# Kernel optimization log

Hardware: AMD Instinct MI355X
Metric: run time of the kernel (lower is better)

Reference implementation:

```python
import jax, jax.numpy as jnp
import numpy as np

NUM_LAYERS = 4
HIDDEN = 32
INPUT = 2
B = 16384
T = 64


def setup_inputs() -> dict:
    key = jax.random.key(0)
    ks = jax.random.split(key, 8)
    s = 1.0 / np.sqrt(HIDDEN)  # PyTorch LSTM default init scale
    return {
        "x": jax.random.normal(ks[0], (B, 3, T), dtype=jnp.float32),
        "W_ih0": jax.random.uniform(ks[1], (4 * HIDDEN, INPUT), minval=-s, maxval=s, dtype=jnp.float32),
        "W_ih": jax.random.uniform(ks[2], (NUM_LAYERS - 1, 4 * HIDDEN, HIDDEN), minval=-s, maxval=s, dtype=jnp.float32),
        "W_hh": jax.random.uniform(ks[3], (NUM_LAYERS, 4 * HIDDEN, HIDDEN), minval=-s, maxval=s, dtype=jnp.float32),
        "b_ih": jax.random.uniform(ks[4], (NUM_LAYERS, 4 * HIDDEN), minval=-s, maxval=s, dtype=jnp.float32),
        "b_hh": jax.random.uniform(ks[5], (NUM_LAYERS, 4 * HIDDEN), minval=-s, maxval=s, dtype=jnp.float32),
        "W_lin": jax.random.uniform(ks[6], (1, HIDDEN), minval=-s, maxval=s, dtype=jnp.float32),
        "b_lin": jax.random.uniform(ks[7], (1,), minval=-s, maxval=s, dtype=jnp.float32),
    }


def _lstm_cell(inp, h, c, Wih, Whh, b):
    # inp: [B, in_dim]; h, c: [B, H]; Wih: [4H, in_dim]; Whh: [4H, H]; b: [4H]
    gates = inp @ Wih.T + h @ Whh.T + b  # [B, 4H]
    i, f, g, o = jnp.split(gates, 4, axis=-1)  # PyTorch gate order: i, f, g, o
    i = jax.nn.sigmoid(i)
    f = jax.nn.sigmoid(f)
    g = jnp.tanh(g)
    o = jax.nn.sigmoid(o)
    c_new = f * c + i * g
    h_new = o * jnp.tanh(c_new)
    return h_new, c_new


def reference(x, W_ih0, W_ih, W_hh, b_ih, b_hh, W_lin, b_lin):
    # x: [B, 3, T]; channel 2 (id) is discarded, as in the original forward.
    feats = x[:, :2, :]                         # [B, 2, T]
    xs = jnp.transpose(feats, (2, 0, 1))        # [T, B, 2]
    bsz = x.shape[0]
    h0 = jnp.zeros((NUM_LAYERS, bsz, HIDDEN), dtype=x.dtype)
    c0 = jnp.zeros((NUM_LAYERS, bsz, HIDDEN), dtype=x.dtype)
    bias = b_ih + b_hh  # [L, 4H]

    def step(carry, xt):
        h, c = carry  # each [L, B, H]
        inp = xt
        hs, cs = [], []
        for l in range(NUM_LAYERS):
            Wih = W_ih0 if l == 0 else W_ih[l - 1]
            h_new, c_new = _lstm_cell(inp, h[l], c[l], Wih, W_hh[l], bias[l])
            hs.append(h_new)
            cs.append(c_new)
            inp = h_new
        return (jnp.stack(hs), jnp.stack(cs)), None

    (h, c), _ = jax.lax.scan(step, (h0, c0), xs)
    # last timestep's top-layer output -> linear -> sigmoid -> squeeze to [B]
    out = jax.nn.sigmoid(h[-1] @ W_lin.T + b_lin)  # [B, 1]
    return out.squeeze(-1)
```

## Files before the change

### kernel.cpp

```cpp
#include <hip/hip_runtime.h>

typedef float  f32x4  __attribute__((ext_vector_type(4)));
typedef short  bf16x8 __attribute__((ext_vector_type(8)));

#define LOG2E      1.4426950408889634f
#define NLOG2E    -1.4426950408889634f
#define NTWOLOG2E -2.8853900817779268f

__device__ __forceinline__ unsigned short f2b(float f) {
    unsigned int u = __builtin_bit_cast(unsigned int, f);
    u += 0x7fffu + ((u >> 16) & 1u);
    return (unsigned short)(u >> 16);
}
__device__ __forceinline__ float b2f(unsigned short s) {
    unsigned int u = ((unsigned int)s) << 16;
    return __builtin_bit_cast(float, u);
}
__device__ __forceinline__ unsigned int pk2(float lo, float hi) {
#if __has_builtin(__builtin_amdgcn_cvt_pk_bf16_f32)
    typedef __bf16 bf16x2 __attribute__((ext_vector_type(2)));
    bf16x2 p = __builtin_amdgcn_cvt_pk_bf16_f32(lo, hi);
    return __builtin_bit_cast(unsigned int, p);
#else
    return (unsigned int)f2b(lo) | ((unsigned int)f2b(hi) << 16);
#endif
}
__device__ __forceinline__ float frcp(float x) { return __builtin_amdgcn_rcpf(x); }
__device__ __forceinline__ float fex2(float x) { return __builtin_amdgcn_exp2f(x); }

__global__ __launch_bounds__(256, 2)
void lstm_mfma(const float* __restrict__ xg,  const float* __restrict__ Wih0,
               const float* __restrict__ Wih, const float* __restrict__ Whh,
               const float* __restrict__ bih, const float* __restrict__ bhh,
               const float* __restrict__ Wlin,const float* __restrict__ blin,
               float* __restrict__ out) {
    __shared__ short        hb[16 * 1280] __attribute__((aligned(16)));
    __shared__ unsigned int xb[64 * 32];

    const int tid  = threadIdx.x;
    const int wv   = __builtin_amdgcn_readfirstlane(tid >> 6);
    const int lane = tid & 63;
    const int m    = lane & 15;
    const int q    = lane >> 4;
    const int row0 = blockIdx.x * 32;

    for (int i = tid; i < 10240; i += 256) ((unsigned int*)hb)[i] = 0u;

    for (int i = tid; i < 2048; i += 256) {
        int r = i >> 6, t = i & 63;
        float x0 = xg[(size_t)(row0 + r) * 192 + t];
        float x1 = xg[(size_t)(row0 + r) * 192 + 64 + t];
        xb[t * 32 + r] = pk2(x0, x1);
    }

    bf16x8 bfr[8][2];
    float  bv[8];
#pragma unroll
    for (int g = 0; g < 8; ++g) {
        const int   T    = g >> 1;
        const int   rowG = T * 32 + 2 * m + (g & 1);
        const float sc   = (T == 2) ? NTWOLOG2E : NLOG2E;
        bv[g] = (bih[wv * 128 + rowG] + bhh[wv * 128 + rowG]) * sc;
#pragma unroll
        for (int c = 0; c < 2; ++c) {
            const int k0 = c * 32 + q * 8;
            float w[8];
            if (wv == 0) {
                if (c == 0) {
#pragma unroll
                    for (int jj = 0; jj < 8; ++jj) w[jj] = 0.0f;
                    if (q == 0) { w[0] = Wih0[rowG * 2]; w[1] = Wih0[rowG * 2 + 1]; }
                } else {
                    const float* src = Whh + rowG * 32 + (k0 - 32);
#pragma unroll
                    for (int jj = 0; jj < 8; ++jj) w[jj] = src[jj];
                }
            } else {
                const float* src = (c == 0) ? (Wih + (wv - 1) * 4096 + rowG * 32 + k0)
                                            : (Whh + wv * 4096 + rowG * 32 + (k0 - 32));
#pragma unroll
                for (int jj = 0; jj < 8; ++jj) w[jj] = src[jj];
            }
            bf16x8 fr;
#pragma unroll
            for (int jj = 0; jj < 8; ++jj) fr[jj] = (short)f2b(w[jj] * sc);
            bfr[g][c] = fr;
        }
    }

    float cst[2][2][4];
#pragma unroll
    for (int tt = 0; tt < 2; ++tt)
#pragma unroll
        for (int hf = 0; hf < 2; ++hf)
#pragma unroll
            for (int r = 0; r < 4; ++r) cst[tt][hf][r] = 0.0f;

    __syncthreads();

    auto cell_step = [&](int t, const short* pa0, const short* pa1, short* hwr) {
        bf16x8 a0[2], a1[2];
#pragma unroll
        for (int tt = 0; tt < 2; ++tt) {
            if (wv == 0) {
                unsigned int xd = xb[t * 32 + tt * 16 + m];
                union { unsigned int u[4]; bf16x8 v; } au;
                au.u[0] = (q == 0) ? xd : 0u; au.u[1] = 0u; au.u[2] = 0u; au.u[3] = 0u;
                a0[tt] = au.v;
            } else {
                a0[tt] = *(const bf16x8*)(pa0 + (tt * 16 + m) * 40 + q * 8);
            }
            a1[tt] = *(const bf16x8*)(pa1 + (tt * 16 + m) * 40 + q * 8);
        }
#pragma unroll
        for (int tt = 0; tt < 2; ++tt) {
            f32x4 acc[8];
#pragma unroll
            for (int g = 0; g < 8; ++g) {
                f32x4 cb = {bv[g], bv[g], bv[g], bv[g]};
                acc[g] = __builtin_amdgcn_mfma_f32_16x16x32_bf16(a0[tt], bfr[g][0], cb, 0, 0, 0);
                acc[g] = __builtin_amdgcn_mfma_f32_16x16x32_bf16(a1[tt], bfr[g][1], acc[g], 0, 0, 0);
            }
            float h0[4];
#pragma unroll
            for (int hf = 0; hf < 2; ++hf) {
#pragma unroll
                for (int r = 0; r < 4; ++r) {
                    float ei = fex2(acc[0 + hf][r]);
                    float ef = fex2(acc[2 + hf][r]);
                    float eg = fex2(acc[4 + hf][r]);
                    float eo = fex2(acc[6 + hf][r]);
                    float ap_f = 1.0f + ef;
                    float p1   = (1.0f + ei) * (1.0f + eg);
                    float R    = frcp(p1 * ap_f);
                    float t1   = (1.0f - eg) * ap_f;
                    float t2   = __builtin_fmaf(cst[tt][hf][r], p1, t1);
                    float cn   = t2 * R;
                    cst[tt][hf][r] = cn;
                    float ec = fex2(cn * NTWOLOG2E);
                    float Rh = frcp((1.0f + eo) * (1.0f + ec));
                    float hh = (1.0f - ec) * Rh;
                    if (hf == 0) {
                        h0[r] = hh;
                    } else {
                        ((unsigned int*)hwr)[(tt * 16 + q * 4 + r) * 20 + m] = pk2(h0[r], hh);
                    }
                }
            }
        }
    };

    for (int S = 0; S < 35; ++S) {
        const int t0 = 2 * (S - wv);
        if (t0 >= 0 && t0 <= 62) {
            const int p  = S & 1;
            const int pb = p ^ 1;
            short*       Lc0 = hb + ((wv * 2 + p ) * 2    ) * 1280;
            short*       Lc1 = Lc0 + 1280;
            const short* Lp1 = hb + ((wv * 2 + pb) * 2 + 1) * 1280;
            const int    lb  = (wv > 0) ? (wv - 1) : 0;
            const short* Dp0 = hb + ((lb * 2 + pb) * 2    ) * 1280;
            const short* Dp1 = Dp0 + 1280;

            cell_step(t0,     Dp0, Lp1, Lc0);
            cell_step(t0 + 1, Dp1, Lc0, Lc1);
        }
        __syncthreads();
    }

    if (tid < 32) {
        const short* h3 = hb + ((3 * 2 + 0) * 2 + 1) * 1280;
        float s = blin[0];
#pragma unroll
        for (int k = 0; k < 32; ++k)
            s += Wlin[k] * b2f((unsigned short)h3[tid * 40 + k]);
        out[row0 + tid] = frcp(1.0f + fex2(s * NLOG2E));
    }
}

extern "C" void kernel_launch(void* const* d_in, const int* in_sizes, int n_in,
                              void* d_out, int out_size, void* d_ws, size_t ws_size,
                              hipStream_t stream) {
    const float* x    = (const float*)d_in[0];
    const float* Wih0 = (const float*)d_in[1];
    const float* Wih  = (const float*)d_in[2];
    const float* Whh  = (const float*)d_in[3];
    const float* bih  = (const float*)d_in[4];
    const float* bhh  = (const float*)d_in[5];
    const float* Wlin = (const float*)d_in[6];
    const float* blin = (const float*)d_in[7];
    float* out = (float*)d_out;

    lstm_mfma<<<512, 256, 0, stream>>>(x, Wih0, Wih, Whh, bih, bhh, Wlin, blin, out);
}
```

Measured before the change: 223.7 us.

## Remap waves to layer pairs and row groups, shortening the wavefront pipeline

Instead of one wave per layer handling all 32 rows, each wave now owns two consecutive layers for one 16-row group (pair P, row group Rg). Layers within a pair run back-to-back inside a wave, so the pipeline has two stages instead of four, which cuts the skewed step count from 35 to 33 and needs less shared memory. Each wave now holds weight fragments for two layers, raising register pressure, and the serial chain per step doubles in length. The c-state exponent scaling is also folded into the g-gate FMA.

```diff
diff --git a/kernel.cpp b/kernel.cpp
--- a/kernel.cpp
+++ b/kernel.cpp
@@ -3,7 +3,7 @@
 typedef float  f32x4  __attribute__((ext_vector_type(4)));
 typedef short  bf16x8 __attribute__((ext_vector_type(8)));
 
-#define LOG2E      1.4426950408889634f
+#define TWOLOG2E   2.8853900817779268f
 #define NLOG2E    -1.4426950408889634f
 #define NTWOLOG2E -2.8853900817779268f
 
@@ -34,17 +34,19 @@
                const float* __restrict__ bih, const float* __restrict__ bhh,
                const float* __restrict__ Wlin,const float* __restrict__ blin,
                float* __restrict__ out) {
-    __shared__ short        hb[16 * 1280] __attribute__((aligned(16)));
+    __shared__ short        hb[12800] __attribute__((aligned(16)));
     __shared__ unsigned int xb[64 * 32];
 
     const int tid  = threadIdx.x;
     const int wv   = __builtin_amdgcn_readfirstlane(tid >> 6);
+    const int P    = wv >> 1;
+    const int Rg   = wv & 1;
     const int lane = tid & 63;
     const int m    = lane & 15;
     const int q    = lane >> 4;
     const int row0 = blockIdx.x * 32;
 
-    for (int i = tid; i < 10240; i += 256) ((unsigned int*)hb)[i] = 0u;
+    for (int i = tid; i < 6400; i += 256) ((unsigned int*)hb)[i] = 0u;
 
     for (int i = tid; i < 2048; i += 256) {
         int r = i >> 6, t = i & 63;
@@ -53,127 +55,134 @@
         xb[t * 32 + r] = pk2(x0, x1);
     }
 
-    bf16x8 bfr[8][2];
-    float  bv[8];
-#pragma unroll
-    for (int g = 0; g < 8; ++g) {
-        const int   T    = g >> 1;
-        const int   rowG = T * 32 + 2 * m + (g & 1);
-        const float sc   = (T == 2) ? NTWOLOG2E : NLOG2E;
-        bv[g] = (bih[wv * 128 + rowG] + bhh[wv * 128 + rowG]) * sc;
-#pragma unroll
-        for (int c = 0; c < 2; ++c) {
-            const int k0 = c * 32 + q * 8;
-            float w[8];
-            if (wv == 0) {
-                if (c == 0) {
-#pragma unroll
-                    for (int jj = 0; jj < 8; ++jj) w[jj] = 0.0f;
-                    if (q == 0) { w[0] = Wih0[rowG * 2]; w[1] = Wih0[rowG * 2 + 1]; }
+    bf16x8 bfr[2][8][2];
+    float  bv[2][8];
+#pragma unroll
+    for (int li = 0; li < 2; ++li) {
+        const int l = 2 * P + li;
+#pragma unroll
+        for (int g = 0; g < 8; ++g) {
+            const int   T    = g >> 1;
+            const int   rowG = T * 32 + 2 * m + (g & 1);
+            const float sc   = (T == 2) ? NTWOLOG2E : NLOG2E;
+            bv[li][g] = (bih[l * 128 + rowG] + bhh[l * 128 + rowG]) * sc;
+#pragma unroll
+            for (int c = 0; c < 2; ++c) {
+                const int k0 = c * 32 + q * 8;
+                float w[8];
+                if (l == 0) {
+                    if (c == 0) {
+#pragma unroll
+                        for (int jj = 0; jj < 8; ++jj) w[jj] = 0.0f;
+                        if (q == 0) { w[0] = Wih0[rowG * 2]; w[1] = Wih0[rowG * 2 + 1]; }
+                    } else {
+                        const float* src = Whh + rowG * 32 + (k0 - 32);
+#pragma unroll
+                        for (int jj = 0; jj < 8; ++jj) w[jj] = src[jj];
+                    }
                 } else {
-                    const float* src = Whh + rowG * 32 + (k0 - 32);
+                    const float* src = (c == 0) ? (Wih + (l - 1) * 4096 + rowG * 32 + k0)
+                                                : (Whh + l * 4096 + rowG * 32 + (k0 - 32));
 #pragma unroll
                     for (int jj = 0; jj < 8; ++jj) w[jj] = src[jj];
                 }
-            } else {
-                const float* src = (c == 0) ? (Wih + (wv - 1) * 4096 + rowG * 32 + k0)
-                                            : (Whh + wv * 4096 + rowG * 32 + (k0 - 32));
-#pragma unroll
-                for (int jj = 0; jj < 8; ++jj) w[jj] = src[jj];
+                bf16x8 fr;
+#pragma unroll
+                for (int jj = 0; jj < 8; ++jj) fr[jj] = (short)f2b(w[jj] * sc);
+                bfr[li][g][c] = fr;
             }
-            bf16x8 fr;
-#pragma unroll
-            for (int jj = 0; jj < 8; ++jj) fr[jj] = (short)f2b(w[jj] * sc);
-            bfr[g][c] = fr;
-        }
-    }
-
-    float cst[2][2][4];
-#pragma unroll
-    for (int tt = 0; tt < 2; ++tt)
+        }
+    }
+
+    float cp[2][2][4];
+#pragma unroll
+    for (int li = 0; li < 2; ++li)
 #pragma unroll
         for (int hf = 0; hf < 2; ++hf)
 #pragma unroll
-            for (int r = 0; r < 4; ++r) cst[tt][hf][r] = 0.0f;
+            for (int r = 0; r < 4; ++r) cp[li][hf][r] = 0.0f;
+
+    short* const h0s0 = hb + Rg * 1280;
+    short* const h0s1 = h0s0 + 640;
+    short* const h2s0 = hb + 7680 + Rg * 1280;
+    short* const h2s1 = h2s0 + 640;
+    short* const h3s0 = hb + 10240 + Rg * 1280;
+    short* const h3s1 = h3s0 + 640;
+    auto h1p = [&](int par, int slot) { return hb + 2560 + ((Rg * 2 + par) * 2 + slot) * 640; };
 
     __syncthreads();
 
-    auto cell_step = [&](int t, const short* pa0, const short* pa1, short* hwr) {
-        bf16x8 a0[2], a1[2];
-#pragma unroll
-        for (int tt = 0; tt < 2; ++tt) {
-            if (wv == 0) {
-                unsigned int xd = xb[t * 32 + tt * 16 + m];
-                union { unsigned int u[4]; bf16x8 v; } au;
-                au.u[0] = (q == 0) ? xd : 0u; au.u[1] = 0u; au.u[2] = 0u; au.u[3] = 0u;
-                a0[tt] = au.v;
-            } else {
-                a0[tt] = *(const bf16x8*)(pa0 + (tt * 16 + m) * 40 + q * 8);
+    auto cell = [&](int li, int xt, const short* pinp, const short* prec, short* pwr) {
+        bf16x8 a0, a1;
+        if (P == 0 && li == 0) {
+            unsigned int xd = xb[xt * 32 + Rg * 16 + m];
+            union { unsigned int u[4]; bf16x8 v; } au;
+            au.u[0] = (q == 0) ? xd : 0u; au.u[1] = 0u; au.u[2] = 0u; au.u[3] = 0u;
+            a0 = au.v;
+        } else {
+            a0 = *(const bf16x8*)(pinp + m * 40 + q * 8);
+        }
+        a1 = *(const bf16x8*)(prec + m * 40 + q * 8);
+
+        f32x4 acc[8];
+#pragma unroll
+        for (int g = 0; g < 8; ++g) {
+            f32x4 cb = {bv[li][g], bv[li][g], bv[li][g], bv[li][g]};
+            acc[g] = __builtin_amdgcn_mfma_f32_16x16x32_bf16(a0, bfr[li][g][0], cb, 0, 0, 0);
+            acc[g] = __builtin_amdgcn_mfma_f32_16x16x32_bf16(a1, bfr[li][g][1], acc[g], 0, 0, 0);
+        }
+        float h0v[4];
+#pragma unroll
+        for (int hf = 0; hf < 2; ++hf) {
+#pragma unroll
+            for (int r = 0; r < 4; ++r) {
+                float ei = fex2(acc[0 + hf][r]);
+                float ef = fex2(acc[2 + hf][r]);
+                float eg = fex2(acc[4 + hf][r]);
+                float eo = fex2(acc[6 + hf][r]);
+                float ap_f = 1.0f + ef;
+                float p1   = (1.0f + ei) * (1.0f + eg);
+                float R_   = frcp(p1 * ap_f);
+                float egp  = __builtin_fmaf(eg, TWOLOG2E, NTWOLOG2E);
+                float t1   = egp * ap_f;
+                float t2   = __builtin_fmaf(cp[li][hf][r], p1, t1);
+                float cn   = t2 * R_;
+                cp[li][hf][r] = cn;
+                float ec = fex2(cn);
+                float Rh = frcp((1.0f + eo) * (1.0f + ec));
+                float hh = (1.0f - ec) * Rh;
+                if (hf == 0) h0v[r] = hh;
+                else ((unsigned int*)pwr)[(q * 4 + r) * 20 + m] = pk2(h0v[r], hh);
             }
-            a1[tt] = *(const bf16x8*)(pa1 + (tt * 16 + m) * 40 + q * 8);
-        }
-#pragma unroll
-        for (int tt = 0; tt < 2; ++tt) {
-            f32x4 acc[8];
-#pragma unroll
-            for (int g = 0; g < 8; ++g) {
-                f32x4 cb = {bv[g], bv[g], bv[g], bv[g]};
-                acc[g] = __builtin_amdgcn_mfma_f32_16x16x32_bf16(a0[tt], bfr[g][0], cb, 0, 0, 0);
-                acc[g] = __builtin_amdgcn_mfma_f32_16x16x32_bf16(a1[tt], bfr[g][1], acc[g], 0, 0, 0);
-            }
-            float h0[4];
-#pragma unroll
-            for (int hf = 0; hf < 2; ++hf) {
-#pragma unroll
-                for (int r = 0; r < 4; ++r) {
-                    float ei = fex2(acc[0 + hf][r]);
-                    float ef = fex2(acc[2 + hf][r]);
-                    float eg = fex2(acc[4 + hf][r]);
-                    float eo = fex2(acc[6 + hf][r]);
-                    float ap_f = 1.0f + ef;
-                    float p1   = (1.0f + ei) * (1.0f + eg);
-                    float R    = frcp(p1 * ap_f);
-                    float t1   = (1.0f - eg) * ap_f;
-                    float t2   = __builtin_fmaf(cst[tt][hf][r], p1, t1);
-                    float cn   = t2 * R;
-                    cst[tt][hf][r] = cn;
-                    float ec = fex2(cn * NTWOLOG2E);
-                    float Rh = frcp((1.0f + eo) * (1.0f + ec));
-                    float hh = (1.0f - ec) * Rh;
-                    if (hf == 0) {
-                        h0[r] = hh;
-                    } else {
-                        ((unsigned int*)hwr)[(tt * 16 + q * 4 + r) * 20 + m] = pk2(h0[r], hh);
-                    }
-                }
-            }
         }
     };
 
-    for (int S = 0; S < 35; ++S) {
-        const int t0 = 2 * (S - wv);
+    for (int S = 0; S < 33; ++S) {
+        const int t0 = 2 * (S - P);
         if (t0 >= 0 && t0 <= 62) {
             const int p  = S & 1;
             const int pb = p ^ 1;
-            short*       Lc0 = hb + ((wv * 2 + p ) * 2    ) * 1280;
-            short*       Lc1 = Lc0 + 1280;
-            const short* Lp1 = hb + ((wv * 2 + pb) * 2 + 1) * 1280;
-            const int    lb  = (wv > 0) ? (wv - 1) : 0;
-            const short* Dp0 = hb + ((lb * 2 + pb) * 2    ) * 1280;
-            const short* Dp1 = Dp0 + 1280;
-
-            cell_step(t0,     Dp0, Lp1, Lc0);
-            cell_step(t0 + 1, Dp1, Lc0, Lc1);
+            if (P == 0) {
+                cell(0, t0,     nullptr,    h0s1,       h0s0);
+                cell(0, t0 + 1, nullptr,    h0s0,       h0s1);
+                cell(1, 0,      h0s0,       h1p(pb, 1), h1p(p, 0));
+                cell(1, 0,      h0s1,       h1p(p, 0),  h1p(p, 1));
+            } else {
+                cell(0, 0,      h1p(pb, 0), h2s1,       h2s0);
+                cell(0, 0,      h1p(pb, 1), h2s0,       h2s1);
+                cell(1, 0,      h2s0,       h3s1,       h3s0);
+                cell(1, 0,      h2s1,       h3s0,       h3s1);
+            }
         }
         __syncthreads();
     }
 
     if (tid < 32) {
-        const short* h3 = hb + ((3 * 2 + 0) * 2 + 1) * 1280;
+        const short* h3 = hb + 10240 + (tid >> 4) * 1280 + 640 + (tid & 15) * 40;
         float s = blin[0];
 #pragma unroll
         for (int k = 0; k < 32; ++k)
-            s += Wlin[k] * b2f((unsigned short)h3[tid * 40 + k]);
+            s += Wlin[k] * b2f((unsigned short)h3[k]);
         out[row0 + tid] = frcp(1.0f + fex2(s * NLOG2E));
     }
 }
```

Result: slower. 427.3 us (+91.1%).

## Replace block barriers with per-wave LDS progress flags in layer wavefront pipeline

Applied to the files above, without the earlier changes.

Swaps the lockstep __syncthreads wavefront schedule for point-to-point sync. Each wave, one per layer, spins on LDS progress counters of its upstream and downstream neighbours before each two-step chunk. The hidden-state buffers become a 4-slot ring per layer, so waves can run ahead of each other. The cell math is also adjusted to fold the 2*log2e scaling into the cell state, removing one multiply before exp2. Spin-waiting on volatile LDS with s_sleep risks extra polling overhead, and correctness depends on the ring slot reuse distance and LDS write ordering.

```diff
diff --git a/kernel.cpp b/kernel.cpp
--- a/kernel.cpp
+++ b/kernel.cpp
@@ -3,7 +3,7 @@
 typedef float  f32x4  __attribute__((ext_vector_type(4)));
 typedef short  bf16x8 __attribute__((ext_vector_type(8)));
 
-#define LOG2E      1.4426950408889634f
+#define TWOLOG2E   2.8853900817779268f
 #define NLOG2E    -1.4426950408889634f
 #define NTWOLOG2E -2.8853900817779268f
 
@@ -36,6 +36,7 @@
                float* __restrict__ out) {
     __shared__ short        hb[16 * 1280] __attribute__((aligned(16)));
     __shared__ unsigned int xb[64 * 32];
+    __shared__ int          prog[4];
 
     const int tid  = threadIdx.x;
     const int wv   = __builtin_amdgcn_readfirstlane(tid >> 6);
@@ -45,6 +46,7 @@
     const int row0 = blockIdx.x * 32;
 
     for (int i = tid; i < 10240; i += 256) ((unsigned int*)hb)[i] = 0u;
+    if (tid < 4) prog[tid] = 0;
 
     for (int i = tid; i < 2048; i += 256) {
         int r = i >> 6, t = i & 63;
@@ -88,13 +90,13 @@
         }
     }
 
-    float cst[2][2][4];
+    float cp[2][2][4];
 #pragma unroll
     for (int tt = 0; tt < 2; ++tt)
 #pragma unroll
         for (int hf = 0; hf < 2; ++hf)
 #pragma unroll
-            for (int r = 0; r < 4; ++r) cst[tt][hf][r] = 0.0f;
+            for (int r = 0; r < 4; ++r) cp[tt][hf][r] = 0.0f;
 
     __syncthreads();
 
@@ -132,48 +134,54 @@
                     float eo = fex2(acc[6 + hf][r]);
                     float ap_f = 1.0f + ef;
                     float p1   = (1.0f + ei) * (1.0f + eg);
-                    float R    = frcp(p1 * ap_f);
-                    float t1   = (1.0f - eg) * ap_f;
-                    float t2   = __builtin_fmaf(cst[tt][hf][r], p1, t1);
-                    float cn   = t2 * R;
-                    cst[tt][hf][r] = cn;
-                    float ec = fex2(cn * NTWOLOG2E);
+                    float R_   = frcp(p1 * ap_f);
+                    float egp  = __builtin_fmaf(eg, TWOLOG2E, NTWOLOG2E);
+                    float t1   = egp * ap_f;
+                    float t2   = __builtin_fmaf(cp[tt][hf][r], p1, t1);
+                    float cn   = t2 * R_;
+                    cp[tt][hf][r] = cn;
+                    float ec = fex2(cn);
                     float Rh = frcp((1.0f + eo) * (1.0f + ec));
                     float hh = (1.0f - ec) * Rh;
-                    if (hf == 0) {
-                        h0[r] = hh;
-                    } else {
-                        ((unsigned int*)hwr)[(tt * 16 + q * 4 + r) * 20 + m] = pk2(h0[r], hh);
-                    }
+                    if (hf == 0) h0[r] = hh;
+                    else ((unsigned int*)hwr)[(tt * 16 + q * 4 + r) * 20 + m] = pk2(h0[r], hh);
                 }
             }
         }
     };
 
-    for (int S = 0; S < 35; ++S) {
-        const int t0 = 2 * (S - wv);
-        if (t0 >= 0 && t0 <= 62) {
-            const int p  = S & 1;
-            const int pb = p ^ 1;
-            short*       Lc0 = hb + ((wv * 2 + p ) * 2    ) * 1280;
-            short*       Lc1 = Lc0 + 1280;
-            const short* Lp1 = hb + ((wv * 2 + pb) * 2 + 1) * 1280;
-            const int    lb  = (wv > 0) ? (wv - 1) : 0;
-            const short* Dp0 = hb + ((lb * 2 + pb) * 2    ) * 1280;
-            const short* Dp1 = Dp0 + 1280;
-
-            cell_step(t0,     Dp0, Lp1, Lc0);
-            cell_step(t0 + 1, Dp1, Lc0, Lc1);
-        }
-        __syncthreads();
-    }
+    volatile int* vp = prog;
+    short* const myBase = hb + wv * 4 * 1280;
+    const short* const inBase = hb + (wv > 0 ? wv - 1 : 0) * 4 * 1280;
+
+    for (int n = 0; n < 32; ++n) {
+        if (wv > 0) { while (vp[wv - 1] < n + 1) __builtin_amdgcn_s_sleep(1); }
+        if (wv < 3) { while (vp[wv + 1] < n - 1) __builtin_amdgcn_s_sleep(1); }
+        asm volatile("" ::: "memory");
+
+        const int t0 = 2 * n;
+        const int s0 = t0 & 3, s1 = (t0 + 1) & 3, sr = (t0 + 3) & 3;
+        short*       w0 = myBase + s0 * 1280;
+        short*       w1 = myBase + s1 * 1280;
+        const short* r0 = myBase + sr * 1280;
+        const short* i0 = inBase + s0 * 1280;
+        const short* i1 = inBase + s1 * 1280;
+
+        cell_step(t0,     i0, r0, w0);
+        cell_step(t0 + 1, i1, w0, w1);
+
+        asm volatile("s_waitcnt lgkmcnt(0)" ::: "memory");
+        if (lane == 0) vp[wv] = n + 1;
+    }
+
+    __syncthreads();
 
     if (tid < 32) {
-        const short* h3 = hb + ((3 * 2 + 0) * 2 + 1) * 1280;
+        const short* h3 = hb + (3 * 4 + 3) * 1280 + tid * 40;
         float s = blin[0];
 #pragma unroll
         for (int k = 0; k < 32; ++k)
-            s += Wlin[k] * b2f((unsigned short)h3[tid * 40 + k]);
+            s += Wlin[k] * b2f((unsigned short)h3[k]);
         out[row0 + tid] = frcp(1.0f + fex2(s * NLOG2E));
     }
 }
```

Measured after the change: 228.1 us. 2.0% more time.
